# Optimization experiments

Measured on AMD Instinct MI355X. Metric: run time of the kernel, lower is better.

Reference implementation:

```python
import jax, jax.numpy as jnp
import numpy as np

G = 8          # group (window) size -> N = G*G = 64
HEADS = 8
DIM = 256
HEAD_DIM = DIM // HEADS
SCALE = HEAD_DIM ** -0.5
POS_DIM = (DIM // 4) // 4  # 16
LN_EPS = 1e-5


def _make_bias_tables():
    # biases: coordinates (1-g..g-1) x (1-g..g-1) -> [(2g-1)^2, 2] float
    r = np.arange(1 - G, G)
    bh, bw = np.meshgrid(r, r, indexing='ij')
    biases = np.stack([bh.ravel(), bw.ravel()], axis=1).astype(np.float32)
    # relative position index [g^2, g^2]
    ch, cw = np.meshgrid(np.arange(G), np.arange(G), indexing='ij')
    coords = np.stack([ch.ravel(), cw.ravel()])              # [2, g^2]
    rel = coords[:, :, None] - coords[:, None, :]            # [2, g^2, g^2]
    rel = rel.transpose(1, 2, 0)
    rel[:, :, 0] += G - 1
    rel[:, :, 1] += G - 1
    rel[:, :, 0] *= 2 * G - 1
    rel_idx = rel.sum(-1).astype(np.int32)                   # [g^2, g^2]
    return biases, rel_idx


def setup_inputs() -> dict:
    key = jax.random.key(0)
    ks = jax.random.split(key, 8)
    B, N, C = 2048, G * G, DIM
    biases_np, rel_idx_np = _make_bias_tables()
    s = lambda fan: 1.0 / np.sqrt(fan)
    return {
        'x': jax.random.normal(ks[0], (B, N, C), jnp.float32),
        'qkv_w': jax.random.normal(ks[1], (C, 3 * C), jnp.float32) * s(C),
        'qkv_b': jnp.zeros((3 * C,), jnp.float32),
        'proj_w': jax.random.normal(ks[2], (C, C), jnp.float32) * s(C),
        'proj_b': jnp.zeros((C,), jnp.float32),
        'pos_proj_w': jax.random.normal(ks[3], (2, POS_DIM), jnp.float32) * s(2),
        'pos_proj_b': jnp.zeros((POS_DIM,), jnp.float32),
        'ln1_g': jnp.ones((POS_DIM,), jnp.float32), 'ln1_b': jnp.zeros((POS_DIM,), jnp.float32),
        'fc1_w': jax.random.normal(ks[4], (POS_DIM, POS_DIM), jnp.float32) * s(POS_DIM),
        'fc1_b': jnp.zeros((POS_DIM,), jnp.float32),
        'ln2_g': jnp.ones((POS_DIM,), jnp.float32), 'ln2_b': jnp.zeros((POS_DIM,), jnp.float32),
        'fc2_w': jax.random.normal(ks[5], (POS_DIM, POS_DIM), jnp.float32) * s(POS_DIM),
        'fc2_b': jnp.zeros((POS_DIM,), jnp.float32),
        'ln3_g': jnp.ones((POS_DIM,), jnp.float32), 'ln3_b': jnp.zeros((POS_DIM,), jnp.float32),
        'fc3_w': jax.random.normal(ks[6], (POS_DIM, HEADS), jnp.float32) * s(POS_DIM),
        'fc3_b': jnp.zeros((HEADS,), jnp.float32),
        'biases': jnp.asarray(biases_np),
        'rel_idx': jnp.asarray(rel_idx_np),
    }


def _ln(h, g, b):
    m = jnp.mean(h, -1, keepdims=True)
    v = jnp.mean((h - m) ** 2, -1, keepdims=True)
    return (h - m) * jax.lax.rsqrt(v + LN_EPS) * g + b


def reference(x, qkv_w, qkv_b, proj_w, proj_b,
              pos_proj_w, pos_proj_b,
              ln1_g, ln1_b, fc1_w, fc1_b,
              ln2_g, ln2_b, fc2_w, fc2_b,
              ln3_g, ln3_b, fc3_w, fc3_b,
              biases, rel_idx):
    B, N, C = x.shape
    # dynamic position bias MLP: [(2g-1)^2, 2] -> [(2g-1)^2, heads]
    h = biases @ pos_proj_w + pos_proj_b
    h = jax.nn.relu(_ln(h, ln1_g, ln1_b)) @ fc1_w + fc1_b
    h = jax.nn.relu(_ln(h, ln2_g, ln2_b)) @ fc2_w + fc2_b
    pos = jax.nn.relu(_ln(h, ln3_g, ln3_b)) @ fc3_w + fc3_b        # [225, H]
    rel_bias = pos[rel_idx]                                        # [N, N, H]
    rel_bias = jnp.transpose(rel_bias, (2, 0, 1))                  # [H, N, N]

    qkv = (x @ qkv_w + qkv_b).reshape(B, N, 3, HEADS, HEAD_DIM)
    qkv = jnp.transpose(qkv, (2, 0, 3, 1, 4))                      # [3, B, H, N, Dh]
    q, k, v = qkv[0] * SCALE, qkv[1], qkv[2]
    attn = jnp.einsum('bhnd,bhmd->bhnm', q, k) + rel_bias[None]    # [B, H, N, N]
    attn = jax.nn.softmax(attn, axis=-1)
    out = jnp.einsum('bhnm,bhmd->bhnd', attn, v)                   # [B, H, N, Dh]
    out = jnp.transpose(out, (0, 2, 1, 3)).reshape(B, N, C)
    return out @ proj_w + proj_b
```

## Files before the change

kernel.cpp:

```cpp
#include <hip/hip_runtime.h>

typedef _Float16 half_t;
typedef __attribute__((ext_vector_type(8))) _Float16 half8;
typedef __attribute__((ext_vector_type(4))) _Float16 half4;
typedef __attribute__((ext_vector_type(4))) float float4v;

#define LN_EPS 1e-5f
#define QK_SCALE 0.17677669529663687f

static __device__ __forceinline__ float4v mfma16(half8 a, half8 b, float4v c) {
    return __builtin_amdgcn_mfma_f32_16x16x32_f16(a, b, c, 0, 0, 0);
}

static __device__ __forceinline__ int swzA(int row, int colByte) {
    return row * 512 + ((((colByte >> 4) ^ ((row >> 1) & 7)) << 4) | (colByte & 15));
}
static __device__ __forceinline__ int swzB(int row, int colByte) {
    return row * 64 + ((((colByte >> 4) ^ ((row >> 1) & 3)) << 4) | (colByte & 15));
}

static __device__ void ln_relu16(float* h, const float* __restrict__ g, const float* __restrict__ b) {
    float m = 0.f;
    for (int j = 0; j < 16; ++j) m += h[j];
    m *= (1.0f / 16.0f);
    float v = 0.f;
    for (int j = 0; j < 16; ++j) { float d = h[j] - m; v += d * d; }
    v *= (1.0f / 16.0f);
    float rs = rsqrtf(v + LN_EPS);
    for (int j = 0; j < 16; ++j) {
        float t = (h[j] - m) * rs * g[j] + b[j];
        h[j] = t > 0.f ? t : 0.f;
    }
}

__global__ void prep_kernel(
    const float* __restrict__ qkv_w,
    const float* __restrict__ proj_w,
    const float* __restrict__ biases,
    const float* __restrict__ pos_w, const float* __restrict__ pos_b,
    const float* __restrict__ ln1_g, const float* __restrict__ ln1_b,
    const float* __restrict__ fc1_w, const float* __restrict__ fc1_b,
    const float* __restrict__ ln2_g, const float* __restrict__ ln2_b,
    const float* __restrict__ fc2_w, const float* __restrict__ fc2_b,
    const float* __restrict__ ln3_g, const float* __restrict__ ln3_b,
    const float* __restrict__ fc3_w, const float* __restrict__ fc3_b,
    const int* __restrict__ rel_idx,
    half_t* __restrict__ wqkvT,
    half_t* __restrict__ wprojT,
    float* __restrict__ rbp)
{
    __shared__ float tile[64][65];
    __shared__ float pos_s[225][8];
    const int t = blockIdx.x;
    const int tid = threadIdx.x;

    if (t < 64) {
        const float* src; half_t* dst; int ncols, rg, cg;
        if (t < 48) { src = qkv_w;  dst = wqkvT;  ncols = 768; rg = t / 12;      cg = t % 12; }
        else        { src = proj_w; dst = wprojT; ncols = 256; rg = (t-48) >> 2; cg = (t-48) & 3; }
        const int r0 = tid >> 6, c = tid & 63;
        for (int i = 0; i < 16; ++i) {
            int r = i * 4 + r0;
            tile[r][c] = src[(rg * 64 + r) * ncols + cg * 64 + c];
        }
        __syncthreads();
        for (int i = 0; i < 16; ++i) {
            int r = i * 4 + r0;
            dst[(cg * 64 + r) * 256 + rg * 64 + c] = (half_t)tile[c][r];
        }
    } else {
        if (tid < 225) {
            float h[16], h2[16];
            float b0 = biases[tid * 2], b1 = biases[tid * 2 + 1];
            for (int j = 0; j < 16; ++j) h[j] = b0 * pos_w[j] + b1 * pos_w[16 + j] + pos_b[j];
            ln_relu16(h, ln1_g, ln1_b);
            for (int j = 0; j < 16; ++j) {
                float s = fc1_b[j];
                for (int k = 0; k < 16; ++k) s += h[k] * fc1_w[k * 16 + j];
                h2[j] = s;
            }
            ln_relu16(h2, ln2_g, ln2_b);
            for (int j = 0; j < 16; ++j) {
                float s = fc2_b[j];
                for (int k = 0; k < 16; ++k) s += h2[k] * fc2_w[k * 16 + j];
                h[j] = s;
            }
            ln_relu16(h, ln3_g, ln3_b);
            for (int j = 0; j < 8; ++j) {
                float s = fc3_b[j];
                for (int k = 0; k < 16; ++k) s += h[k] * fc3_w[k * 8 + j];
                pos_s[tid][j] = s;
            }
        }
        __syncthreads();
        for (int e = tid; e < 8 * 64 * 64; e += 256) {
            int hh = e >> 12, rem = e & 4095;
            int row = rem >> 6, c = rem & 63;
            int tj = c >> 4, mm = c & 15;
            rbp[hh * 4096 + row * 64 + mm * 4 + tj] = pos_s[rel_idx[row * 64 + c]][hh];
        }
    }
}

__global__ __launch_bounds__(512, 2) void fused_kernel(
    const float* __restrict__ x,
    const half_t* __restrict__ wqkvT,
    const float* __restrict__ qkv_b,
    const half_t* __restrict__ wprojT,
    const float* __restrict__ proj_b,
    const float* __restrict__ rbp,
    float* __restrict__ out)
{
    __shared__ __align__(16) char smem[81920];
    char* xs  = smem;
    char* atn = smem + 32768;
    char* scr = smem + 65536;

    const int b   = blockIdx.x;
    const int tid = threadIdx.x;
    const int w    = tid >> 6;
    const int lane = tid & 63;
    const int m = lane & 15;
    const int g = lane >> 4;
    char* wscr   = scr + w * 2048;
    char* parena = xs  + w * 4096;

    const float* xg = x + (size_t)b * 16384;
    #pragma unroll
    for (int i = 0; i < 8; ++i) {
        int u = tid + i * 512;
        int row = u >> 6, c4 = u & 63;
        float4v xv = *(const float4v*)(xg + u * 4);
        half4 hv;
        hv[0] = (half_t)xv[0]; hv[1] = (half_t)xv[1];
        hv[2] = (half_t)xv[2]; hv[3] = (half_t)xv[3];
        *(half4*)(xs + swzA(row, c4 * 8)) = hv;
    }
    __syncthreads();

    half8 aq[4], bk[4];
    #pragma unroll
    for (int pt = 0; pt < 2; ++pt) {
        const int wrow0 = pt * 256 + w * 32;
        float4v acc[2][4];
        #pragma unroll
        for (int c2 = 0; c2 < 2; ++c2)
            #pragma unroll
            for (int ti = 0; ti < 4; ++ti) acc[c2][ti] = {0.f, 0.f, 0.f, 0.f};
        #pragma unroll
        for (int kk = 0; kk < 8; ++kk) {
            half8 wf0 = *(const half8*)(wqkvT + (size_t)(wrow0 +      m) * 256 + kk * 32 + g * 8);
            half8 wf1 = *(const half8*)(wqkvT + (size_t)(wrow0 + 16 + m) * 256 + kk * 32 + g * 8);
            #pragma unroll
            for (int ti = 0; ti < 4; ++ti) {
                half8 af = *(const half8*)(xs + swzA(ti * 16 + m, kk * 64 + g * 16));
                acc[0][ti] = mfma16(wf0, af, acc[0][ti]);
                acc[1][ti] = mfma16(wf1, af, acc[1][ti]);
            }
        }
        half4 pk[2][4];
        #pragma unroll
        for (int c2 = 0; c2 < 2; ++c2) {
            #pragma unroll
            for (int ti = 0; ti < 4; ++ti)
                #pragma unroll
                for (int r = 0; r < 4; ++r)
                    pk[c2][ti][r] = (half_t)(acc[c2][ti][r] + qkv_b[wrow0 + c2 * 16 + g * 4 + r]);
        }
        #pragma unroll
        for (int ti = 0; ti < 4; ++ti) {
            *(half4*)(wscr + swzB(m, (g * 4) * 2))        = pk[0][ti];
            *(half4*)(wscr + swzB(m, (16 + g * 4) * 2))   = pk[1][ti];
            half8 fr = *(const half8*)(wscr + swzB(m, g * 16));
            if (pt == 0) aq[ti] = fr; else bk[ti] = fr;
        }
    }

    float rinv[4][4];
    half4 ph[4][4];
    const float* rbh = rbp + w * 4096;
    #pragma unroll
    for (int ti = 0; ti < 4; ++ti) {
        float4v z = {0.f, 0.f, 0.f, 0.f};
        float4v s0 = mfma16(aq[ti], bk[0], z);
        float4v s1 = mfma16(aq[ti], bk[1], z);
        float4v s2 = mfma16(aq[ti], bk[2], z);
        float4v s3 = mfma16(aq[ti], bk[3], z);
        float4v rb[4];
        #pragma unroll
        for (int r = 0; r < 4; ++r)
            rb[r] = *(const float4v*)(rbh + (ti * 16 + g * 4 + r) * 64 + m * 4);
        #pragma unroll
        for (int r = 0; r < 4; ++r) {
            float v0 = s0[r] * QK_SCALE + rb[r][0];
            float v1 = s1[r] * QK_SCALE + rb[r][1];
            float v2 = s2[r] * QK_SCALE + rb[r][2];
            float v3 = s3[r] * QK_SCALE + rb[r][3];
            float mx = fmaxf(fmaxf(v0, v1), fmaxf(v2, v3));
            mx = fmaxf(mx, __shfl_xor(mx, 1));
            mx = fmaxf(mx, __shfl_xor(mx, 2));
            mx = fmaxf(mx, __shfl_xor(mx, 4));
            mx = fmaxf(mx, __shfl_xor(mx, 8));
            float e0 = __expf(v0 - mx), e1 = __expf(v1 - mx);
            float e2 = __expf(v2 - mx), e3 = __expf(v3 - mx);
            float s = e0 + e1 + e2 + e3;
            s += __shfl_xor(s, 1); s += __shfl_xor(s, 2);
            s += __shfl_xor(s, 4); s += __shfl_xor(s, 8);
            rinv[ti][r] = 1.0f / s;
            ph[ti][0][r] = (half_t)e0;
            ph[ti][1][r] = (half_t)e1;
            ph[ti][2][r] = (half_t)e2;
            ph[ti][3][r] = (half_t)e3;
        }
    }

    half4 vh[2][4];
    {
        const int wrow0 = 512 + w * 32;
        float4v acc[2][4];
        #pragma unroll
        for (int c2 = 0; c2 < 2; ++c2)
            #pragma unroll
            for (int ti = 0; ti < 4; ++ti) acc[c2][ti] = {0.f, 0.f, 0.f, 0.f};
        #pragma unroll
        for (int kk = 0; kk < 8; ++kk) {
            half8 wf0 = *(const half8*)(wqkvT + (size_t)(wrow0 +      m) * 256 + kk * 32 + g * 8);
            half8 wf1 = *(const half8*)(wqkvT + (size_t)(wrow0 + 16 + m) * 256 + kk * 32 + g * 8);
            #pragma unroll
            for (int ti = 0; ti < 4; ++ti) {
                half8 af = *(const half8*)(xs + swzA(ti * 16 + m, kk * 64 + g * 16));
                acc[0][ti] = mfma16(af, wf0, acc[0][ti]);
                acc[1][ti] = mfma16(af, wf1, acc[1][ti]);
            }
        }
        float vb0 = qkv_b[wrow0 + m], vb1 = qkv_b[wrow0 + 16 + m];
        #pragma unroll
        for (int c2 = 0; c2 < 2; ++c2)
            #pragma unroll
            for (int ti = 0; ti < 4; ++ti)
                #pragma unroll
                for (int r = 0; r < 4; ++r)
                    vh[c2][ti][r] = (half_t)(acc[c2][ti][r] + (c2 ? vb1 : vb0));
    }
    __syncthreads();

    float4v oacc[2][4];
    #pragma unroll
    for (int tjd = 0; tjd < 2; ++tjd)
        #pragma unroll
        for (int ti = 0; ti < 4; ++ti) oacc[tjd][ti] = {0.f, 0.f, 0.f, 0.f};
    #pragma unroll
    for (int nc = 0; nc < 2; ++nc) {
        #pragma unroll
        for (int ti = 0; ti < 4; ++ti)
            #pragma unroll
            for (int t2 = 0; t2 < 2; ++t2)
                #pragma unroll
                for (int r = 0; r < 4; ++r)
                    *(half_t*)(parena + swzB(ti * 16 + g * 4 + r, (t2 * 16 + m) * 2)) =
                        ph[ti][nc * 2 + t2][r];
        #pragma unroll
        for (int c2 = 0; c2 < 2; ++c2)
            #pragma unroll
            for (int t2 = 0; t2 < 2; ++t2)
                *(half4*)(wscr + swzB(c2 * 16 + m, (t2 * 16 + g * 4) * 2)) = vh[c2][nc * 2 + t2];
        half8 bv0 = *(const half8*)(wscr + swzB(m, g * 16));
        half8 bv1 = *(const half8*)(wscr + swzB(16 + m, g * 16));
        #pragma unroll
        for (int ti = 0; ti < 4; ++ti) {
            half8 pa = *(const half8*)(parena + swzB(ti * 16 + m, g * 16));
            oacc[0][ti] = mfma16(pa, bv0, oacc[0][ti]);
            oacc[1][ti] = mfma16(pa, bv1, oacc[1][ti]);
        }
    }
    #pragma unroll
    for (int tjd = 0; tjd < 2; ++tjd)
        #pragma unroll
        for (int ti = 0; ti < 4; ++ti)
            #pragma unroll
            for (int r = 0; r < 4; ++r) {
                float val = oacc[tjd][ti][r] * rinv[ti][r];
                *(half_t*)(atn + swzA(ti * 16 + g * 4 + r, (w * 32 + tjd * 16 + m) * 2)) = (half_t)val;
            }
    __syncthreads();

    float* og = out + (size_t)b * 16384;
    const int oc0 = w * 32;
    float4v pacc[2][4];
    #pragma unroll
    for (int c2 = 0; c2 < 2; ++c2)
        #pragma unroll
        for (int ti = 0; ti < 4; ++ti) pacc[c2][ti] = {0.f, 0.f, 0.f, 0.f};
    #pragma unroll
    for (int kk = 0; kk < 8; ++kk) {
        half8 wf0 = *(const half8*)(wprojT + (size_t)(oc0 +      m) * 256 + kk * 32 + g * 8);
        half8 wf1 = *(const half8*)(wprojT + (size_t)(oc0 + 16 + m) * 256 + kk * 32 + g * 8);
        #pragma unroll
        for (int ti = 0; ti < 4; ++ti) {
            half8 af = *(const half8*)(atn + swzA(ti * 16 + m, kk * 64 + g * 16));
            pacc[0][ti] = mfma16(af, wf0, pacc[0][ti]);
            pacc[1][ti] = mfma16(af, wf1, pacc[1][ti]);
        }
    }
    float pb0 = proj_b[oc0 + m], pb1 = proj_b[oc0 + 16 + m];
    #pragma unroll
    for (int c2 = 0; c2 < 2; ++c2)
        #pragma unroll
        for (int ti = 0; ti < 4; ++ti)
            #pragma unroll
            for (int r = 0; r < 4; ++r)
                og[(ti * 16 + g * 4 + r) * 256 + oc0 + c2 * 16 + m] =
                    pacc[c2][ti][r] + (c2 ? pb1 : pb0);
}

extern "C" void kernel_launch(void* const* d_in, const int* in_sizes, int n_in,
                              void* d_out, int out_size, void* d_ws, size_t ws_size,
                              hipStream_t stream) {
    const float* x          = (const float*)d_in[0];
    const float* qkv_w      = (const float*)d_in[1];
    const float* qkv_b      = (const float*)d_in[2];
    const float* proj_w     = (const float*)d_in[3];
    const float* proj_b     = (const float*)d_in[4];
    const float* pos_proj_w = (const float*)d_in[5];
    const float* pos_proj_b = (const float*)d_in[6];
    const float* ln1_g = (const float*)d_in[7];
    const float* ln1_b = (const float*)d_in[8];
    const float* fc1_w = (const float*)d_in[9];
    const float* fc1_b = (const float*)d_in[10];
    const float* ln2_g = (const float*)d_in[11];
    const float* ln2_b = (const float*)d_in[12];
    const float* fc2_w = (const float*)d_in[13];
    const float* fc2_b = (const float*)d_in[14];
    const float* ln3_g = (const float*)d_in[15];
    const float* ln3_b = (const float*)d_in[16];
    const float* fc3_w = (const float*)d_in[17];
    const float* fc3_b = (const float*)d_in[18];
    const float* biases = (const float*)d_in[19];
    const int*  rel_idx = (const int*)d_in[20];

    half_t* wqkvT  = (half_t*)d_ws;
    half_t* wprojT = (half_t*)((char*)d_ws + 393216);
    float*  rbp    = (float*)((char*)d_ws + 524288);

    const int B = in_sizes[0] / (64 * 256);

    prep_kernel<<<65, 256, 0, stream>>>(qkv_w, proj_w, biases, pos_proj_w, pos_proj_b,
                                        ln1_g, ln1_b, fc1_w, fc1_b,
                                        ln2_g, ln2_b, fc2_w, fc2_b,
                                        ln3_g, ln3_b, fc3_w, fc3_b,
                                        rel_idx, wqkvT, wprojT, rbp);
    fused_kernel<<<B, 512, 0, stream>>>(x, wqkvT, qkv_b, wprojT, proj_b, rbp,
                                        (float*)d_out);
}
```

Baseline: 284.7 us.

## Shrink shared memory to 64KB by aliasing buffers and normalizing softmax early

```diff
diff --git a/kernel.cpp b/kernel.cpp
--- a/kernel.cpp
+++ b/kernel.cpp
@@ -111,10 +111,10 @@
     const float* __restrict__ rbp,
     float* __restrict__ out)
 {
-    __shared__ __align__(16) char smem[81920];
+    __shared__ __align__(16) char smem[65536];
     char* xs  = smem;
-    char* atn = smem + 32768;
-    char* scr = smem + 65536;
+    char* atn = smem;
+    char* scr = smem + 32768;
 
     const int b   = blockIdx.x;
     const int tid = threadIdx.x;
@@ -122,8 +122,7 @@
     const int lane = tid & 63;
     const int m = lane & 15;
     const int g = lane >> 4;
-    char* wscr   = scr + w * 2048;
-    char* parena = xs  + w * 4096;
+    char* wscr = scr + w * 4096;
 
     const float* xg = x + (size_t)b * 16384;
     #pragma unroll
@@ -176,7 +175,6 @@
         }
     }
 
-    float rinv[4][4];
     half4 ph[4][4];
     const float* rbh = rbp + w * 4096;
     #pragma unroll
@@ -206,11 +204,11 @@
             float s = e0 + e1 + e2 + e3;
             s += __shfl_xor(s, 1); s += __shfl_xor(s, 2);
             s += __shfl_xor(s, 4); s += __shfl_xor(s, 8);
-            rinv[ti][r] = 1.0f / s;
-            ph[ti][0][r] = (half_t)e0;
-            ph[ti][1][r] = (half_t)e1;
-            ph[ti][2][r] = (half_t)e2;
-            ph[ti][3][r] = (half_t)e3;
+            float is = 1.0f / s;
+            ph[ti][0][r] = (half_t)(e0 * is);
+            ph[ti][1][r] = (half_t)(e1 * is);
+            ph[ti][2][r] = (half_t)(e2 * is);
+            ph[ti][3][r] = (half_t)(e3 * is);
         }
     }
 
@@ -257,8 +255,13 @@
             for (int t2 = 0; t2 < 2; ++t2)
                 #pragma unroll
                 for (int r = 0; r < 4; ++r)
-                    *(half_t*)(parena + swzB(ti * 16 + g * 4 + r, (t2 * 16 + m) * 2)) =
+                    *(half_t*)(wscr + swzB(ti * 16 + g * 4 + r, (t2 * 16 + m) * 2)) =
                         ph[ti][nc * 2 + t2][r];
+        half8 pa[4];
+        #pragma unroll
+        for (int ti = 0; ti < 4; ++ti)
+            pa[ti] = *(const half8*)(wscr + swzB(ti * 16 + m, g * 16));
+        __builtin_amdgcn_sched_barrier(0);
         #pragma unroll
         for (int c2 = 0; c2 < 2; ++c2)
             #pragma unroll
@@ -268,9 +271,8 @@
         half8 bv1 = *(const half8*)(wscr + swzB(16 + m, g * 16));
         #pragma unroll
         for (int ti = 0; ti < 4; ++ti) {
-            half8 pa = *(const half8*)(parena + swzB(ti * 16 + m, g * 16));
-            oacc[0][ti] = mfma16(pa, bv0, oacc[0][ti]);
-            oacc[1][ti] = mfma16(pa, bv1, oacc[1][ti]);
+            oacc[0][ti] = mfma16(pa[ti], bv0, oacc[0][ti]);
+            oacc[1][ti] = mfma16(pa[ti], bv1, oacc[1][ti]);
         }
     }
     #pragma unroll
@@ -278,10 +280,9 @@
         #pragma unroll
         for (int ti = 0; ti < 4; ++ti)
             #pragma unroll
-            for (int r = 0; r < 4; ++r) {
-                float val = oacc[tjd][ti][r] * rinv[ti][r];
-                *(half_t*)(atn + swzA(ti * 16 + g * 4 + r, (w * 32 + tjd * 16 + m) * 2)) = (half_t)val;
-            }
+            for (int r = 0; r < 4; ++r)
+                *(half_t*)(atn + swzA(ti * 16 + g * 4 + r, (w * 32 + tjd * 16 + m) * 2)) =
+                    (half_t)oacc[tjd][ti][r];
     __syncthreads();
 
     float* og = out + (size_t)b * 16384;
```

Result: no change. 287.9 us (+1.1%).
